# Kernel optimization log

Measured on AMD Instinct MI355X. Metric: run time of the kernel, lower is better.

Reference implementation:

```python
import jax, jax.numpy as jnp
import numpy as np

B, S, D = 4, 1024, 2048
H = 16
DH = D // H  # 128
SCALE = float(DH) ** 0.5  # faithful to source: scores / head_dim**(-0.5) == scores * sqrt(head_dim)


def setup_inputs() -> dict:
    key = jax.random.key(0)
    ks = jax.random.split(key, 5)
    std = 0.02
    return {
        "x": jax.random.normal(ks[0], (B, S, D), dtype=jnp.float32),
        "Wq": jax.random.normal(ks[1], (D, D), dtype=jnp.float32) * std,
        "Wk": jax.random.normal(ks[2], (D, D), dtype=jnp.float32) * std,
        "Wv": jax.random.normal(ks[3], (D, D), dtype=jnp.float32) * std,
        "Wo": jax.random.normal(ks[4], (D, D), dtype=jnp.float32) * std,
    }


def reference(x, Wq, Wk, Wv, Wo):
    b, s, _ = x.shape
    # torch Linear: y = x @ W.T  (weights stored [out, in]); no bias (qkv_bias=False)
    q = jnp.einsum('bsd,ed->bse', x, Wq).reshape(b, s, H, DH)
    k = jnp.einsum('bsd,ed->bse', x, Wk).reshape(b, s, H, DH)
    v = jnp.einsum('bsd,ed->bse', x, Wv).reshape(b, s, H, DH)
    # [b, h, q, k] scores
    scores = jnp.einsum('bqhd,bkhd->bhqk', q, k)
    causal = jnp.triu(jnp.ones((s, s), dtype=bool), k=1)  # True above diagonal -> masked
    scores = jnp.where(causal, -jnp.inf, scores)
    attn = jax.nn.softmax(scores * jnp.asarray(SCALE, scores.dtype), axis=-1)
    # dropout p=0.0 -> identity
    ctx = jnp.einsum('bhqk,bkhd->bqhd', attn, v).reshape(b, s, D)
    return jnp.einsum('bsd,ed->bse', ctx, Wo)
```

## Files before the change

kernel.cpp:

```cpp
#include <hip/hip_runtime.h>


typedef _Float16 f16;
typedef _Float16 f16x8 __attribute__((ext_vector_type(8)));
typedef _Float16 f16x4 __attribute__((ext_vector_type(4)));
typedef float f32x4 __attribute__((ext_vector_type(4)));

__device__ __forceinline__ f32x4 mfma16(f16x8 a, f16x8 b, f32x4 c) {
  return __builtin_amdgcn_mfma_f32_16x16x32_f16(a, b, c, 0, 0, 0);
}

__device__ __forceinline__ void gld16(const void* g, void* l) {
  __builtin_amdgcn_global_load_lds(
      (const __attribute__((address_space(1))) void*)g,
      (__attribute__((address_space(3))) void*)l, 16, 0, 0);
}

__global__ void conv_plain_k(const float* __restrict__ src, f16* __restrict__ dst, int n4) {
  int i = blockIdx.x * 256 + threadIdx.x;
  if (i >= n4) return;
  float4 v = reinterpret_cast<const float4*>(src)[i];
  f16x4 h;
  h[0] = (f16)v.x; h[1] = (f16)v.y; h[2] = (f16)v.z; h[3] = (f16)v.w;
  reinterpret_cast<f16x4*>(dst)[i] = h;
}

template<int OUTMODE>
__global__ __launch_bounds__(256, 2) void gemm_bt(
    const f16* __restrict__ Ah, const f16* __restrict__ Bh,
    void* __restrict__ C0, int Nn, int Kk)
{
  __shared__ f16 sAh[128 * 32];
  __shared__ f16 sBh[128 * 32];

  const int t = threadIdx.x;
  const int wave = t >> 6, lane = t & 63;
  const int l15 = lane & 15, lg = lane >> 4;
  const int wr = wave >> 1, wc = wave & 1;
  const long m0 = (long)blockIdx.y * 128, n0 = (long)blockIdx.x * 128;

  const int srow = t >> 2;
  const int scol = (t & 3) * 8;
  const long aoff = (m0 + srow) * (long)Kk + scol;
  const long boff = (n0 + srow) * (long)Kk + scol;
  const long rowstep = 64L * Kk;
  const int ldst = wave * 512;

  f32x4 acc[4][4] = {};
  const int lof = l15 * 32 + lg * 8;

  for (int k0 = 0; k0 < Kk; k0 += 32) {
    gld16(Ah + aoff + k0,           sAh + ldst);
    gld16(Ah + aoff + rowstep + k0, sAh + 2048 + ldst);
    gld16(Bh + boff + k0,           sBh + ldst);
    gld16(Bh + boff + rowstep + k0, sBh + 2048 + ldst);
    __syncthreads();
    f16x8 a_h[4], b_h[4];
#pragma unroll
    for (int i = 0; i < 4; ++i) a_h[i] = *(const f16x8*)(sAh + (wr * 64 + i * 16) * 32 + lof);
#pragma unroll
    for (int j = 0; j < 4; ++j) b_h[j] = *(const f16x8*)(sBh + (wc * 64 + j * 16) * 32 + lof);
#pragma unroll
    for (int i = 0; i < 4; ++i)
#pragma unroll
      for (int j = 0; j < 4; ++j)
        acc[i][j] = mfma16(a_h[i], b_h[j], acc[i][j]);
    __syncthreads();
  }

#pragma unroll
  for (int i = 0; i < 4; ++i)
#pragma unroll
    for (int j = 0; j < 4; ++j)
#pragma unroll
      for (int r = 0; r < 4; ++r) {
        long row = m0 + wr * 64 + i * 16 + lg * 4 + r;
        long col = n0 + wc * 64 + j * 16 + l15;
        long idx = row * Nn + col;
        float v = acc[i][j][r];
        if constexpr (OUTMODE == 0) {
          ((f16*)C0)[idx] = (f16)v;
        } else {
          ((float*)C0)[idx] = v;
        }
      }
}

__global__ void transpose_v_k(const f16* __restrict__ V, f16* __restrict__ Vt) {
  const int st = blockIdx.x;
  const int dt = blockIdx.y;
  const int bh = blockIdx.z;
  const int b = bh >> 4, h = bh & 15;
  __shared__ f16 tile[64][68];
  const int t = threadIdx.x;
  const int r = t >> 4;
  const int c4 = (t & 15) * 4;
#pragma unroll
  for (int p = 0; p < 4; ++p) {
    int row = r + p * 16;
    f16x4 v = *(const f16x4*)(V + (long)(b * 1024 + st * 64 + row) * 2048 + h * 128 + dt * 64 + c4);
    tile[row][c4] = v[0]; tile[row][c4 + 1] = v[1];
    tile[row][c4 + 2] = v[2]; tile[row][c4 + 3] = v[3];
  }
  __syncthreads();
#pragma unroll
  for (int p = 0; p < 4; ++p) {
    int drow = r + p * 16;
    f16x4 o;
    o[0] = tile[c4][drow]; o[1] = tile[c4 + 1][drow];
    o[2] = tile[c4 + 2][drow]; o[3] = tile[c4 + 3][drow];
    *(f16x4*)(Vt + ((long)bh * 128 + dt * 64 + drow) * 1024 + st * 64 + c4) = o;
  }
}

__global__ __launch_bounds__(256, 4) void attn_k(
    const f16* __restrict__ Qh, const f16* __restrict__ Kh,
    const f16* __restrict__ Vt, f16* __restrict__ Ctx)
{
  const int g = blockIdx.x;
  const int p = blockIdx.y;
  const int b = g & 3, h = g >> 2;
  const int t = threadIdx.x, wave = t >> 6, lane = t & 63;
  const int l15 = lane & 15, lg = lane >> 4;

  __shared__ f16 sKh[64 * 128];
  __shared__ f16 sV [128 * 64];
  __shared__ f16 pbuf[4][16 * 72];

  const long kbase = (long)(b * 1024) * 2048 + h * 128;
  const long vtb = (long)((b * 16 + h) * 128) * 1024;
  const float SC2 = (float)(11.313708498984761 * 1.4426950408889634);

  const int krow_s = t >> 4;
  const int vrow_s = t >> 3;

#pragma unroll
  for (int half = 0; half < 2; ++half) {
    const int myqt = half ? p : 15 - p;
    const int qbase = myqt * 64 + wave * 16;

    f16x8 q_h[4];
#pragma unroll
    for (int c = 0; c < 4; ++c) {
      long o8 = (long)(b * 1024 + qbase + l15) * 2048 + h * 128 + c * 32 + lg * 8;
      q_h[c] = *(const f16x8*)(Qh + o8);
    }

    float mm[4], ll[4];
#pragma unroll
    for (int r = 0; r < 4; ++r) { mm[r] = -1e30f; ll[r] = 0.f; }
    f32x4 o[8] = {};

    const int nt = myqt + 1;
    for (int kt = 0; kt < nt; ++kt) {
      const int k0 = kt * 64;
#pragma unroll
      for (int q = 0; q < 4; ++q) {
        const int row = q * 16 + krow_s;
        const int colx = ((t & 15) * 8) ^ ((row & 7) << 3);
        gld16(Kh + kbase + (long)(k0 + row) * 2048 + colx, sKh + q * 2048 + t * 8);
      }
#pragma unroll
      for (int q = 0; q < 4; ++q) {
        const int row = q * 32 + vrow_s;
        const int colx = ((t & 7) * 8) ^ ((row & 7) << 3);
        gld16(Vt + vtb + (long)row * 1024 + k0 + colx, sV + q * 2048 + t * 8);
      }
      __syncthreads();

      f32x4 s[4] = {};
#pragma unroll
      for (int c = 0; c < 4; ++c)
#pragma unroll
        for (int j = 0; j < 4; ++j) {
          const int krow = j * 16 + l15;
          const int koff = krow * 128 + (((c * 32 + lg * 8)) ^ ((krow & 7) << 3));
          f16x8 kh = *(const f16x8*)(sKh + koff);
          s[j] = mfma16(q_h[c], kh, s[j]);
        }

      if (k0 + 63 > qbase) {
        const int qrow = qbase + lg * 4;
#pragma unroll
        for (int j = 0; j < 4; ++j) {
          const int kcol = k0 + j * 16 + l15;
#pragma unroll
          for (int r = 0; r < 4; ++r)
            if (kcol > qrow + r) s[j][r] = -1e30f;
        }
      }
#pragma unroll
      for (int j = 0; j < 4; ++j)
        s[j] = s[j] * SC2;

#pragma unroll
      for (int r = 0; r < 4; ++r) {
        float tm = fmaxf(fmaxf(s[0][r], s[1][r]), fmaxf(s[2][r], s[3][r]));
        tm = fmaxf(tm, __shfl_xor(tm, 1));
        tm = fmaxf(tm, __shfl_xor(tm, 2));
        tm = fmaxf(tm, __shfl_xor(tm, 4));
        tm = fmaxf(tm, __shfl_xor(tm, 8));
        float mn = fmaxf(mm[r], tm);
        float fac = __builtin_amdgcn_exp2f(mm[r] - mn);
        mm[r] = mn;
        float rs = 0.f;
#pragma unroll
        for (int j = 0; j < 4; ++j) {
          float pv = __builtin_amdgcn_exp2f(s[j][r] - mn);
          rs += pv;
          pbuf[wave][(lg * 4 + r) * 72 + j * 16 + l15] = (f16)pv;
        }
        rs += __shfl_xor(rs, 1);
        rs += __shfl_xor(rs, 2);
        rs += __shfl_xor(rs, 4);
        rs += __shfl_xor(rs, 8);
        ll[r] = ll[r] * fac + rs;
#pragma unroll
        for (int n = 0; n < 8; ++n) o[n][r] *= fac;
      }
      __syncthreads();

#pragma unroll
      for (int kc = 0; kc < 2; ++kc) {
        f16x8 pa = *(const f16x8*)(&pbuf[wave][l15 * 72 + kc * 32 + lg * 8]);
#pragma unroll
        for (int n = 0; n < 8; ++n) {
          const int vrow = n * 16 + l15;
          f16x8 vv = *(const f16x8*)(sV + vrow * 64 + (((kc * 32 + lg * 8)) ^ ((vrow & 7) << 3)));
          o[n] = mfma16(pa, vv, o[n]);
        }
      }
      __syncthreads();
    }

#pragma unroll
    for (int r = 0; r < 4; ++r) {
      float inv = 1.0f / ll[r];
      long rbase = (long)(b * 1024 + qbase + lg * 4 + r) * 2048 + h * 128;
#pragma unroll
      for (int n = 0; n < 8; ++n)
        Ctx[rbase + n * 16 + l15] = (f16)(o[n][r] * inv);
    }
  }
}

extern "C" void kernel_launch(void* const* d_in, const int* in_sizes, int n_in,
                              void* d_out, int out_size, void* d_ws, size_t ws_size,
                              hipStream_t stream) {
  (void)in_sizes; (void)n_in; (void)out_size; (void)ws_size;
  const float* x  = (const float*)d_in[0];
  const float* Wq = (const float*)d_in[1];
  const float* Wk = (const float*)d_in[2];
  const float* Wv = (const float*)d_in[3];
  const float* Wo = (const float*)d_in[4];
  float* out = (float*)d_out;
  f16* ws = (f16*)d_ws;

  const long MD = 4096L * 2048;
  const long DD = 2048L * 2048;

  f16* xh = ws;
  f16* wq = ws + MD;
  f16* wk = wq + DD;
  f16* wv = wk + DD;
  f16* wo = wv + DD;
  f16* qh = wo + DD;
  f16* kh = qh + MD;
  f16* vh = kh + MD;
  f16* vt = vh + MD;
  f16* ctx = xh;

  conv_plain_k<<<8192, 256, 0, stream>>>(x,  xh, (int)(MD / 4));
  conv_plain_k<<<4096, 256, 0, stream>>>(Wq, wq, (int)(DD / 4));
  conv_plain_k<<<4096, 256, 0, stream>>>(Wk, wk, (int)(DD / 4));
  conv_plain_k<<<4096, 256, 0, stream>>>(Wv, wv, (int)(DD / 4));
  conv_plain_k<<<4096, 256, 0, stream>>>(Wo, wo, (int)(DD / 4));

  dim3 gg(16, 32);
  gemm_bt<0><<<gg, 256, 0, stream>>>(xh, wq, qh, 2048, 2048);
  gemm_bt<0><<<gg, 256, 0, stream>>>(xh, wk, kh, 2048, 2048);
  gemm_bt<0><<<gg, 256, 0, stream>>>(xh, wv, vh, 2048, 2048);
  transpose_v_k<<<dim3(16, 2, 64), 256, 0, stream>>>(vh, vt);
  attn_k<<<dim3(64, 8), 256, 0, stream>>>(qh, kh, vt, ctx);
  gemm_bt<2><<<gg, 256, 0, stream>>>(ctx, wo, out, 2048, 2048);
}
```

Before: 394.2 us.

## Fuse QKV projections into one 256x256 double-buffered GEMM and add lazy softmax rescale

```diff
diff --git a/kernel.cpp b/kernel.cpp
--- a/kernel.cpp
+++ b/kernel.cpp
@@ -15,6 +15,14 @@
       (const __attribute__((address_space(1))) void*)g,
       (__attribute__((address_space(3))) void*)l, 16, 0, 0);
 }
+
+#define BAR() __builtin_amdgcn_s_barrier()
+#define VMCNT0() asm volatile("s_waitcnt vmcnt(0)" ::: "memory")
+#define LGKM0()                                        \
+  do {                                                 \
+    asm volatile("s_waitcnt lgkmcnt(0)" ::: "memory"); \
+    __builtin_amdgcn_sched_barrier(0);                 \
+  } while (0)
 
 __global__ void conv_plain_k(const float* __restrict__ src, f16* __restrict__ dst, int n4) {
   int i = blockIdx.x * 256 + threadIdx.x;
@@ -23,6 +31,147 @@
   f16x4 h;
   h[0] = (f16)v.x; h[1] = (f16)v.y; h[2] = (f16)v.z; h[3] = (f16)v.w;
   reinterpret_cast<f16x4*>(dst)[i] = h;
+}
+
+__global__ __launch_bounds__(512, 1) void qkv_gemm(
+    const f16* __restrict__ A, const f16* __restrict__ Wcat,
+    f16* __restrict__ Out, int Kk)
+{
+  __shared__ f16 sA[2][256 * 64];
+  __shared__ f16 sB[2][256 * 64];
+
+  const int t = threadIdx.x;
+  const int wave = t >> 6, lane = t & 63;
+  const int l15 = lane & 15, lg = lane >> 4;
+  const int wr = wave >> 2, wc = wave & 3;
+  const long m0 = (long)blockIdx.y * 256;
+  const long n0 = (long)blockIdx.x * 256;
+
+  const int crow = t >> 3;
+  const int cf = ((((t & 7) * 16) ^ ((crow & 7) << 4)) >> 1);
+  const f16* gA = A    + (m0 + crow) * (long)Kk + cf;
+  const f16* gB = Wcat + (n0 + crow) * (long)Kk + cf;
+  const long rq = 64L * Kk;
+  const int dsb = t * 8;
+
+  const int xorb = (l15 & 7) << 4;
+  const int ac0 = ((lg * 16) ^ xorb) >> 1;
+  const int ac1 = (((lg * 16) + 64) ^ xorb) >> 1;
+
+  f32x4 acc[8][4] = {};
+
+  const int NT = Kk >> 6;
+
+#pragma unroll
+  for (int q = 0; q < 4; ++q) gld16(gA + q * rq, &sA[0][q * 4096 + dsb]);
+#pragma unroll
+  for (int q = 0; q < 4; ++q) gld16(gB + q * rq, &sB[0][q * 4096 + dsb]);
+  VMCNT0();
+  BAR();
+
+  for (int kt = 0; kt < NT; ++kt) {
+    const int c = kt & 1;
+    const f16* pA = &sA[c][0];
+    const f16* pB = &sB[c][0];
+    const long gofs = (long)(kt + 1) * 64;
+
+    f16x8 b0[4], a0[4];
+#pragma unroll
+    for (int n = 0; n < 4; ++n) {
+      const int row = wc * 64 + n * 16 + l15;
+      b0[n] = *(const f16x8*)(pB + row * 64 + ac0);
+    }
+#pragma unroll
+    for (int m = 0; m < 4; ++m) {
+      const int row = wr * 128 + m * 16 + l15;
+      a0[m] = *(const f16x8*)(pA + row * 64 + ac0);
+    }
+    if (kt + 1 < NT) {
+#pragma unroll
+      for (int q = 0; q < 4; ++q) gld16(gA + gofs + q * rq, &sA[c ^ 1][q * 4096 + dsb]);
+#pragma unroll
+      for (int q = 0; q < 4; ++q) gld16(gB + gofs + q * rq, &sB[c ^ 1][q * 4096 + dsb]);
+    }
+    BAR();
+    LGKM0();
+    __builtin_amdgcn_s_setprio(1);
+#pragma unroll
+    for (int m = 0; m < 4; ++m)
+#pragma unroll
+      for (int n = 0; n < 4; ++n)
+        acc[m][n] = mfma16(a0[m], b0[n], acc[m][n]);
+    __builtin_amdgcn_s_setprio(0);
+    BAR();
+
+    f16x8 a1[4];
+#pragma unroll
+    for (int m = 0; m < 4; ++m) {
+      const int row = wr * 128 + 64 + m * 16 + l15;
+      a1[m] = *(const f16x8*)(pA + row * 64 + ac0);
+    }
+    BAR();
+    LGKM0();
+    __builtin_amdgcn_s_setprio(1);
+#pragma unroll
+    for (int m = 0; m < 4; ++m)
+#pragma unroll
+      for (int n = 0; n < 4; ++n)
+        acc[4 + m][n] = mfma16(a1[m], b0[n], acc[4 + m][n]);
+    __builtin_amdgcn_s_setprio(0);
+    BAR();
+
+    f16x8 b1[4], a2[4];
+#pragma unroll
+    for (int n = 0; n < 4; ++n) {
+      const int row = wc * 64 + n * 16 + l15;
+      b1[n] = *(const f16x8*)(pB + row * 64 + ac1);
+    }
+#pragma unroll
+    for (int m = 0; m < 4; ++m) {
+      const int row = wr * 128 + m * 16 + l15;
+      a2[m] = *(const f16x8*)(pA + row * 64 + ac1);
+    }
+    BAR();
+    LGKM0();
+    __builtin_amdgcn_s_setprio(1);
+#pragma unroll
+    for (int m = 0; m < 4; ++m)
+#pragma unroll
+      for (int n = 0; n < 4; ++n)
+        acc[m][n] = mfma16(a2[m], b1[n], acc[m][n]);
+    __builtin_amdgcn_s_setprio(0);
+    BAR();
+
+    f16x8 a3[4];
+#pragma unroll
+    for (int m = 0; m < 4; ++m) {
+      const int row = wr * 128 + 64 + m * 16 + l15;
+      a3[m] = *(const f16x8*)(pA + row * 64 + ac1);
+    }
+    BAR();
+    LGKM0();
+    __builtin_amdgcn_s_setprio(1);
+#pragma unroll
+    for (int m = 0; m < 4; ++m)
+#pragma unroll
+      for (int n = 0; n < 4; ++n)
+        acc[4 + m][n] = mfma16(a3[m], b1[n], acc[4 + m][n]);
+    __builtin_amdgcn_s_setprio(0);
+    if (kt + 1 < NT) VMCNT0();
+    BAR();
+  }
+
+  f16* base = Out + (long)(n0 >> 11) * (4096L * 2048);
+  const int lc0 = (int)(n0 & 2047) + wc * 64;
+#pragma unroll
+  for (int m = 0; m < 8; ++m)
+#pragma unroll
+    for (int n = 0; n < 4; ++n)
+#pragma unroll
+      for (int r = 0; r < 4; ++r) {
+        const long grow = m0 + wr * 128 + m * 16 + lg * 4 + r;
+        base[grow * 2048 + lc0 + n * 16 + l15] = (f16)acc[m][n][r];
+      }
 }
 
 template<int OUTMODE>
@@ -200,13 +349,18 @@
         tm = fmaxf(tm, __shfl_xor(tm, 2));
         tm = fmaxf(tm, __shfl_xor(tm, 4));
         tm = fmaxf(tm, __shfl_xor(tm, 8));
-        float mn = fmaxf(mm[r], tm);
-        float fac = __builtin_amdgcn_exp2f(mm[r] - mn);
-        mm[r] = mn;
+        if (!__all(tm - mm[r] <= 8.0f)) {
+          float mn = fmaxf(mm[r], tm);
+          float fac = __builtin_amdgcn_exp2f(mm[r] - mn);
+          mm[r] = mn;
+          ll[r] *= fac;
+#pragma unroll
+          for (int n = 0; n < 8; ++n) o[n][r] *= fac;
+        }
         float rs = 0.f;
 #pragma unroll
         for (int j = 0; j < 4; ++j) {
-          float pv = __builtin_amdgcn_exp2f(s[j][r] - mn);
+          float pv = __builtin_amdgcn_exp2f(s[j][r] - mm[r]);
           rs += pv;
           pbuf[wave][(lg * 4 + r) * 72 + j * 16 + l15] = (f16)pv;
         }
@@ -214,9 +368,7 @@
         rs += __shfl_xor(rs, 2);
         rs += __shfl_xor(rs, 4);
         rs += __shfl_xor(rs, 8);
-        ll[r] = ll[r] * fac + rs;
-#pragma unroll
-        for (int n = 0; n < 8; ++n) o[n][r] *= fac;
+        ll[r] += rs;
       }
       __syncthreads();
 
@@ -276,11 +428,8 @@
   conv_plain_k<<<4096, 256, 0, stream>>>(Wv, wv, (int)(DD / 4));
   conv_plain_k<<<4096, 256, 0, stream>>>(Wo, wo, (int)(DD / 4));
 
-  dim3 gg(16, 32);
-  gemm_bt<0><<<gg, 256, 0, stream>>>(xh, wq, qh, 2048, 2048);
-  gemm_bt<0><<<gg, 256, 0, stream>>>(xh, wk, kh, 2048, 2048);
-  gemm_bt<0><<<gg, 256, 0, stream>>>(xh, wv, vh, 2048, 2048);
+  qkv_gemm<<<dim3(24, 16), 512, 0, stream>>>(xh, wq, qh, 2048);
   transpose_v_k<<<dim3(16, 2, 64), 256, 0, stream>>>(vh, vt);
   attn_k<<<dim3(64, 8), 256, 0, stream>>>(qh, kh, vt, ctx);
-  gemm_bt<2><<<gg, 256, 0, stream>>>(ctx, wo, out, 2048, 2048);
-}
+  gemm_bt<2><<<dim3(16, 32), 256, 0, stream>>>(ctx, wo, out, 2048, 2048);
+}
```

Result: no change. 387.8 us (-1.6%).
